# Kernel tuning notes

Measured on AMD Instinct MI355X. Metric: run time of the kernel, lower is better.

Reference implementation:

```python
import jax, jax.numpy as jnp
import numpy as np

N_NODES = 100000
N_GRAPHS = 512
HID = 128
IN_DIM = 128
OUT_DIM = 10
N_EDGES = 1600000


def gcn_conv(x, src, dst, W, b, n):
    # PyG GCNConv: add self-loops, symmetric normalization D^-1/2 (A+I) D^-1/2, then linear.
    h = x @ W  # [N, H]
    deg = jnp.zeros((n,), h.dtype).at[dst].add(1.0) + 1.0  # +1 self-loop
    dinv = jax.lax.rsqrt(deg)
    norm = dinv[src] * dinv[dst]  # [E]
    agg = jnp.zeros_like(h).at[dst].add(h[src] * norm[:, None])
    agg = agg + h * (dinv * dinv)[:, None]  # self-loop messages
    return agg + b


def setup_inputs() -> dict:
    key = jax.random.key(0)
    ks = jax.random.split(key, 12)
    x = jax.random.normal(ks[0], (N_NODES, IN_DIM), jnp.float32)
    edge_index = jax.random.randint(ks[1], (2, N_EDGES), 0, N_NODES)
    batch = jnp.sort(jax.random.randint(ks[2], (N_NODES,), 0, N_GRAPHS))
    def lin(k, fan_in, shape):
        bound = 1.0 / np.sqrt(fan_in)
        return jax.random.uniform(k, shape, jnp.float32, -bound, bound)
    W1 = lin(ks[3], IN_DIM, (IN_DIM, HID)); b1 = lin(ks[4], IN_DIM, (HID,))
    W2 = lin(ks[5], HID, (HID, HID)); b2 = lin(ks[6], HID, (HID,))
    W3 = lin(ks[7], HID, (HID, HID)); b3 = lin(ks[8], HID, (HID,))
    Wc1 = lin(ks[9], 2 * HID, (2 * HID, HID)); bc1 = lin(ks[9], 2 * HID, (HID,))
    Wc2 = lin(ks[10], HID, (HID, OUT_DIM)); bc2 = lin(ks[11], HID, (OUT_DIM,))
    return {"x": x, "edge_index": edge_index, "batch": batch,
            "W1": W1, "b1": b1, "W2": W2, "b2": b2, "W3": W3, "b3": b3,
            "Wc1": Wc1, "bc1": bc1, "Wc2": Wc2, "bc2": bc2}


def reference(x, edge_index, batch, W1, b1, W2, b2, W3, b3, Wc1, bc1, Wc2, bc2):
    src, dst = edge_index[0], edge_index[1]
    n = x.shape[0]
    h = jax.nn.relu(gcn_conv(x, src, dst, W1, b1, n))
    h = jax.nn.relu(gcn_conv(h, src, dst, W2, b2, n))
    h = gcn_conv(h, src, dst, W3, b3, n)  # no relu after last conv
    # global mean pool
    sums = jax.ops.segment_sum(h, batch, num_segments=N_GRAPHS)
    cnt = jax.ops.segment_sum(jnp.ones((n,), h.dtype), batch, num_segments=N_GRAPHS)
    mean = sums / jnp.maximum(cnt, 1.0)[:, None]
    # global max pool
    mx = jax.ops.segment_max(h, batch, num_segments=N_GRAPHS)
    mx = jnp.where(jnp.isfinite(mx), mx, 0.0)
    g = jnp.concatenate([mean, mx], axis=1)  # [G, 2H]
    g = jax.nn.relu(g @ Wc1 + bc1)
    return g @ Wc2 + bc2
```

## Files before the change

kernel.cpp:

```cpp
#include <hip/hip_runtime.h>

#define H 128
#define CAP 64
#define CSRB 4096

typedef __attribute__((ext_vector_type(8))) short bf16x8;
typedef __attribute__((ext_vector_type(4))) float f32x4;

__device__ __forceinline__ unsigned short f2bf(float f) {
  unsigned u = __float_as_uint(f);
  unsigned r = u + 0x7FFFu + ((u >> 16) & 1u);
  return (unsigned short)(r >> 16);
}
__device__ __forceinline__ float bf2f(unsigned short s) {
  return __uint_as_float(((unsigned)s) << 16);
}

__global__ __launch_bounds__(256) void fat_setup_csr(
    const int* __restrict__ src, const int* __restrict__ dst,
    int* __restrict__ cursor, int* __restrict__ csr_src,
    int ne, int range,
    const float* __restrict__ x,
    const float* __restrict__ W1, const float* __restrict__ W2, const float* __restrict__ W3,
    unsigned short* __restrict__ Xb, unsigned short* __restrict__ Wt,
    int n, int totalX4) {
  if (blockIdx.x < CSRB) {
    int r = blockIdx.x & 7;
    int slice = blockIdx.x >> 3;
    const int slices = CSRB / 8;
    int ne4 = ne / 4;
    int chunk4 = (ne4 + slices - 1) / slices;
    int beg4 = slice * chunk4;
    int end4 = beg4 + chunk4; if (end4 > ne4) end4 = ne4;
    int lo = r * range;
    int hi = lo + range;
    for (int e4 = beg4 + threadIdx.x; e4 < end4; e4 += 256) {
      int e = e4 * 4;
      int4 d = *(const int4*)(dst + e);
      if (d.x >= lo && d.x < hi) { int p = atomicAdd(&cursor[d.x], 1); if (p < CAP) csr_src[(size_t)d.x * CAP + p] = src[e + 0]; }
      if (d.y >= lo && d.y < hi) { int p = atomicAdd(&cursor[d.y], 1); if (p < CAP) csr_src[(size_t)d.y * CAP + p] = src[e + 1]; }
      if (d.z >= lo && d.z < hi) { int p = atomicAdd(&cursor[d.z], 1); if (p < CAP) csr_src[(size_t)d.z * CAP + p] = src[e + 2]; }
      if (d.w >= lo && d.w < hi) { int p = atomicAdd(&cursor[d.w], 1); if (p < CAP) csr_src[(size_t)d.w * CAP + p] = src[e + 3]; }
    }
    if (r == 0 && slice == 0) {
      int base = ne4 * 4;
      int t = base + threadIdx.x;
      if (t < ne) {
        int d = dst[t];
        int p = atomicAdd(&cursor[d], 1);
        if (p < CAP) csr_src[(size_t)d * CAP + p] = src[t];
      }
    }
    return;
  }
  long long i = (long long)(blockIdx.x - CSRB) * 256 + threadIdx.x;
  if (i < totalX4) {
    float4 v = *(const float4*)(x + i * 4);
    ushort4 o;
    o.x = f2bf(v.x); o.y = f2bf(v.y); o.z = f2bf(v.z); o.w = f2bf(v.w);
    *(ushort4*)(Xb + i * 4) = o;
    return;
  }
  i -= totalX4;
  if (i < 3 * H * H) {
    int w = (int)(i >> 14);
    int rem = (int)i & (H * H - 1);
    int c = rem >> 7;
    int k = rem & 127;
    const float* W = (w == 0) ? W1 : (w == 1) ? W2 : W3;
    Wt[i] = f2bf(W[(size_t)k * H + c]);
  }
}

__global__ void dinv_gstart(const int* __restrict__ deg, float* __restrict__ dinv,
                            const int* __restrict__ batch, int* __restrict__ g_start,
                            int n, int G) {
  int i = blockIdx.x * blockDim.x + threadIdx.x;
  if (i >= n) return;
  dinv[i] = rsqrtf((float)(deg[i] + 1));
  int b = batch[i];
  int prev = (i == 0) ? -1 : batch[i - 1];
  for (int g = prev + 1; g <= b; ++g) g_start[g] = i;
  if (i == n - 1) {
    for (int g = b + 1; g <= G; ++g) g_start[g] = n;
  }
}

#define SWLD 136
__global__ __launch_bounds__(256) void gemm_mfma(
    const unsigned short* __restrict__ Ab, const unsigned short* __restrict__ Wt,
    const float* __restrict__ dinv, unsigned short* __restrict__ outb, int n) {
  __shared__ unsigned short sW[H * SWLD];
  int tid = threadIdx.x;
  {
    int c = tid >> 1, hh = tid & 1;
    const int4* s = (const int4*)(Wt + (size_t)c * H + hh * 64);
    int4* d = (int4*)(sW + (size_t)c * SWLD + hh * 64);
#pragma unroll
    for (int i = 0; i < 8; ++i) d[i] = s[i];
  }
  __syncthreads();

  int wave = tid >> 6;
  int lane = tid & 63;
  int m = lane & 15;
  int quad = lane >> 4;
  int row = blockIdx.x * 64 + wave * 16 + m;
  bool rv = row < n;

  f32x4 acc[8];
#pragma unroll
  for (int t = 0; t < 8; ++t) acc[t] = (f32x4){0.f, 0.f, 0.f, 0.f};

  const unsigned short* arow = Ab + (size_t)(rv ? row : 0) * H;
#pragma unroll
  for (int k0 = 0; k0 < H; k0 += 32) {
    bf16x8 af;
    if (rv) af = *(const bf16x8*)(arow + k0 + quad * 8);
    else    af = (bf16x8){0, 0, 0, 0, 0, 0, 0, 0};
#pragma unroll
    for (int ct = 0; ct < 8; ++ct) {
      bf16x8 bfr = *(const bf16x8*)(sW + (size_t)(ct * 16 + m) * SWLD + k0 + quad * 8);
      acc[ct] = __builtin_amdgcn_mfma_f32_16x16x32_bf16(af, bfr, acc[ct], 0, 0, 0);
    }
  }

  int orow0 = blockIdx.x * 64 + wave * 16 + quad * 4;
#pragma unroll
  for (int r = 0; r < 4; ++r) {
    int orow = orow0 + r;
    if (orow < n) {
      float dv = dinv[orow];
      unsigned short* o = outb + (size_t)orow * H + m;
#pragma unroll
      for (int ct = 0; ct < 8; ++ct) o[ct * 16] = f2bf(acc[ct][r] * dv);
    }
  }
}

template <bool RELU, bool OUTF32>
__global__ __launch_bounds__(256) void aggregate_bf(
    const unsigned short* __restrict__ hs, const int* __restrict__ deg,
    const int* __restrict__ csr_src, const float* __restrict__ dinv,
    const float* __restrict__ b, void* __restrict__ outv, int n) {
  int node = blockIdx.x * 8 + (threadIdx.x >> 5);
  if (node >= n) return;
  int c = (threadIdx.x & 31) << 2;
  int dg = deg[node];
  int beg  = node * CAP;
  int end8 = beg + (dg & ~7);
  int end  = beg + dg;

  ushort4 sv = *(const ushort4*)(hs + (size_t)node * H + c);
  float4 acc;
  acc.x = bf2f(sv.x); acc.y = bf2f(sv.y); acc.z = bf2f(sv.z); acc.w = bf2f(sv.w);

  for (int k = beg; k < end8; k += 8) {
    int4 ca = *(const int4*)(csr_src + k);
    int4 cb = *(const int4*)(csr_src + k + 4);
    ushort4 v0 = *(const ushort4*)(hs + (size_t)ca.x * H + c);
    ushort4 v1 = *(const ushort4*)(hs + (size_t)ca.y * H + c);
    ushort4 v2 = *(const ushort4*)(hs + (size_t)ca.z * H + c);
    ushort4 v3 = *(const ushort4*)(hs + (size_t)ca.w * H + c);
    ushort4 v4 = *(const ushort4*)(hs + (size_t)cb.x * H + c);
    ushort4 v5 = *(const ushort4*)(hs + (size_t)cb.y * H + c);
    ushort4 v6 = *(const ushort4*)(hs + (size_t)cb.z * H + c);
    ushort4 v7 = *(const ushort4*)(hs + (size_t)cb.w * H + c);
    acc.x += ((bf2f(v0.x) + bf2f(v1.x)) + (bf2f(v2.x) + bf2f(v3.x))) +
             ((bf2f(v4.x) + bf2f(v5.x)) + (bf2f(v6.x) + bf2f(v7.x)));
    acc.y += ((bf2f(v0.y) + bf2f(v1.y)) + (bf2f(v2.y) + bf2f(v3.y))) +
             ((bf2f(v4.y) + bf2f(v5.y)) + (bf2f(v6.y) + bf2f(v7.y)));
    acc.z += ((bf2f(v0.z) + bf2f(v1.z)) + (bf2f(v2.z) + bf2f(v3.z))) +
             ((bf2f(v4.z) + bf2f(v5.z)) + (bf2f(v6.z) + bf2f(v7.z)));
    acc.w += ((bf2f(v0.w) + bf2f(v1.w)) + (bf2f(v2.w) + bf2f(v3.w))) +
             ((bf2f(v4.w) + bf2f(v5.w)) + (bf2f(v6.w) + bf2f(v7.w)));
  }
  for (int k = end8; k < end; ++k) {
    int s = csr_src[k];
    ushort4 v = *(const ushort4*)(hs + (size_t)s * H + c);
    acc.x += bf2f(v.x); acc.y += bf2f(v.y);
    acc.z += bf2f(v.z); acc.w += bf2f(v.w);
  }

  float dv = dinv[node];
  float4 bb = *(const float4*)(b + c);
  float4 o;
  o.x = fmaf(acc.x, dv, bb.x);
  o.y = fmaf(acc.y, dv, bb.y);
  o.z = fmaf(acc.z, dv, bb.z);
  o.w = fmaf(acc.w, dv, bb.w);
  if (RELU) {
    o.x = fmaxf(o.x, 0.f); o.y = fmaxf(o.y, 0.f);
    o.z = fmaxf(o.z, 0.f); o.w = fmaxf(o.w, 0.f);
  }
  if (OUTF32) {
    *(float4*)((float*)outv + (size_t)node * H + c) = o;
  } else {
    ushort4 ob;
    ob.x = f2bf(o.x); ob.y = f2bf(o.y); ob.z = f2bf(o.z); ob.w = f2bf(o.w);
    *(ushort4*)((unsigned short*)outv + (size_t)node * H + c) = ob;
  }
}

__global__ __launch_bounds__(256) void pool2(
    const float* __restrict__ h, const int* __restrict__ g_start,
    float* __restrict__ gmean, float* __restrict__ gmax, int n) {
  __shared__ float ssum[16][64];
  __shared__ float smax[16][64];
  int g = blockIdx.x >> 1;
  int half = blockIdx.x & 1;
  int beg = g_start[g];
  int end = g_start[g + 1];
  int q = threadIdx.x >> 4;
  int c = (threadIdx.x & 15) << 2;
  int cg = half * 64 + c;

  float4 s = make_float4(0.f, 0.f, 0.f, 0.f);
  float4 m = make_float4(-INFINITY, -INFINITY, -INFINITY, -INFINITY);
  for (int node = beg + q; node < end; node += 16) {
    float4 v = *(const float4*)(h + (size_t)node * H + cg);
    s.x += v.x; s.y += v.y; s.z += v.z; s.w += v.w;
    m.x = fmaxf(m.x, v.x); m.y = fmaxf(m.y, v.y);
    m.z = fmaxf(m.z, v.z); m.w = fmaxf(m.w, v.w);
  }
  *(float4*)&ssum[q][c] = s;
  *(float4*)&smax[q][c] = m;
  __syncthreads();

  int cnt = end - beg;
  int t = threadIdx.x;
  if (t < 64) {
    float tot = 0.f;
#pragma unroll
    for (int qq = 0; qq < 16; ++qq) tot += ssum[qq][t];
    gmean[(size_t)g * H + half * 64 + t] = tot / fmaxf((float)cnt, 1.0f);
  } else if (t < 128) {
    int cc = t - 64;
    float mx = -INFINITY;
#pragma unroll
    for (int qq = 0; qq < 16; ++qq) mx = fmaxf(mx, smax[qq][cc]);
    gmax[(size_t)g * H + half * 64 + cc] = (cnt == 0) ? 0.0f : mx;
  }
}

__global__ __launch_bounds__(128) void classify_kernel(
    const float* __restrict__ gmean, const float* __restrict__ gmax,
    const float* __restrict__ Wc1, const float* __restrict__ bc1,
    const float* __restrict__ Wc2, const float* __restrict__ bc2,
    float* __restrict__ out) {
  __shared__ float gv[2 * H];
  __shared__ float hid[H];
  int gid = blockIdx.x;
  int t = threadIdx.x;
  gv[t] = gmean[(size_t)gid * H + t];
  gv[H + t] = gmax[(size_t)gid * H + t];
  __syncthreads();
  float acc = 0.f;
#pragma unroll 8
  for (int k = 0; k < 2 * H; ++k) acc = fmaf(gv[k], Wc1[(size_t)k * H + t], acc);
  hid[t] = fmaxf(acc + bc1[t], 0.f);
  __syncthreads();
  if (t < 10) {
    float a2 = 0.f;
    for (int j = 0; j < H; ++j) a2 = fmaf(hid[j], Wc2[(size_t)j * 10 + t], a2);
    out[(size_t)gid * 10 + t] = a2 + bc2[t];
  }
}

extern "C" void kernel_launch(void* const* d_in, const int* in_sizes, int n_in,
                              void* d_out, int out_size, void* d_ws, size_t ws_size,
                              hipStream_t stream) {
  const float* x    = (const float*)d_in[0];
  const int* ei     = (const int*)d_in[1];
  const int* batch  = (const int*)d_in[2];
  const float* W1   = (const float*)d_in[3];
  const float* b1   = (const float*)d_in[4];
  const float* W2   = (const float*)d_in[5];
  const float* b2   = (const float*)d_in[6];
  const float* W3   = (const float*)d_in[7];
  const float* b3   = (const float*)d_in[8];
  const float* Wc1  = (const float*)d_in[9];
  const float* bc1  = (const float*)d_in[10];
  const float* Wc2  = (const float*)d_in[11];
  const float* bc2  = (const float*)d_in[12];
  float* out = (float*)d_out;

  const int n  = in_sizes[2];
  const int ne = in_sizes[1] / 2;
  const int G  = 512;
  const size_t NFb = (size_t)n * H;

  const int* src = ei;
  const int* dst = ei + ne;

  unsigned short* P_bf = (unsigned short*)d_ws;
  unsigned short* Q_bf = P_bf + NFb;
  float*          F2f  = (float*)(Q_bf + NFb);
  unsigned short* Xb   = (unsigned short*)F2f;
  int* csr_src = (int*)(F2f + NFb);
  const size_t csr_cap = (size_t)n * CAP;
  char* p = (char*)(csr_src + csr_cap);
  int*            cursor   = (int*)p;            p += (size_t)n * 4;
  float*          dinv     = (float*)p;          p += (size_t)n * 4;
  int*            g_start  = (int*)p;            p += (size_t)(G + 1) * 4;
  float*          gmean    = (float*)p;          p += (size_t)G * H * 4;
  float*          gmax     = (float*)p;          p += (size_t)G * H * 4;
  p = (char*)(((uintptr_t)p + 255) & ~(uintptr_t)255);
  unsigned short* Wt       = (unsigned short*)p; p += (size_t)3 * H * H * 2;

  hipMemsetAsync(cursor, 0, (size_t)n * 4, stream);

  {
    int totalX4 = n * H / 4;
    long long setup_items = (long long)totalX4 + 3 * H * H;
    int setup_blocks = (int)((setup_items + 255) / 256);
    int range = (n + 7) / 8;
    fat_setup_csr<<<CSRB + setup_blocks, 256, 0, stream>>>(
        src, dst, cursor, csr_src, ne, range,
        x, W1, W2, W3, Xb, Wt, n, totalX4);
  }
  dinv_gstart<<<(n + 255) / 256, 256, 0, stream>>>(cursor, dinv, batch, g_start, n, G);

  const int tile_grid = (n + 63) / 64;
  const int node_grid = (n + 7) / 8;

  gemm_mfma<<<tile_grid, 256, 0, stream>>>(Xb, Wt, dinv, Q_bf, n);
  aggregate_bf<true, false><<<node_grid, 256, 0, stream>>>(Q_bf, cursor, csr_src, dinv, b1, P_bf, n);

  gemm_mfma<<<tile_grid, 256, 0, stream>>>(P_bf, Wt + H * H, dinv, Q_bf, n);
  aggregate_bf<true, false><<<node_grid, 256, 0, stream>>>(Q_bf, cursor, csr_src, dinv, b2, P_bf, n);

  gemm_mfma<<<tile_grid, 256, 0, stream>>>(P_bf, Wt + 2 * H * H, dinv, Q_bf, n);
  aggregate_bf<false, true><<<node_grid, 256, 0, stream>>>(Q_bf, cursor, csr_src, dinv, b3, F2f, n);

  pool2<<<2 * G, 256, 0, stream>>>(F2f, g_start, gmean, gmax, n);
  classify_kernel<<<G, 128, 0, stream>>>(gmean, gmax, Wc1, bc1, Wc2, bc2, out);
}
```

Baseline: 464.6 us.

## Drop dinv/g_start kernel and fuse pooling with classifier

Removes the dinv_gstart kernel. dinv is now recomputed inline from the degree array with rsqrtf in the GEMM epilogue and in the aggregation kernel. Graph boundaries are found by binary search over the sorted batch array. Pooling and the classifier MLP are merged into one kernel per graph, so there are two fewer launches and no gmean/gmax round-trip through global memory. In exchange, one block now covers all 128 channels of a graph instead of two half-blocks, and the classifier uses only half of the threads.

```diff
diff --git a/kernel.cpp b/kernel.cpp
--- a/kernel.cpp
+++ b/kernel.cpp
@@ -72,24 +72,10 @@
   }
 }
 
-__global__ void dinv_gstart(const int* __restrict__ deg, float* __restrict__ dinv,
-                            const int* __restrict__ batch, int* __restrict__ g_start,
-                            int n, int G) {
-  int i = blockIdx.x * blockDim.x + threadIdx.x;
-  if (i >= n) return;
-  dinv[i] = rsqrtf((float)(deg[i] + 1));
-  int b = batch[i];
-  int prev = (i == 0) ? -1 : batch[i - 1];
-  for (int g = prev + 1; g <= b; ++g) g_start[g] = i;
-  if (i == n - 1) {
-    for (int g = b + 1; g <= G; ++g) g_start[g] = n;
-  }
-}
-
 #define SWLD 136
 __global__ __launch_bounds__(256) void gemm_mfma(
     const unsigned short* __restrict__ Ab, const unsigned short* __restrict__ Wt,
-    const float* __restrict__ dinv, unsigned short* __restrict__ outb, int n) {
+    const int* __restrict__ deg, unsigned short* __restrict__ outb, int n) {
   __shared__ unsigned short sW[H * SWLD];
   int tid = threadIdx.x;
   {
@@ -130,7 +116,7 @@
   for (int r = 0; r < 4; ++r) {
     int orow = orow0 + r;
     if (orow < n) {
-      float dv = dinv[orow];
+      float dv = rsqrtf((float)(deg[orow] + 1));
       unsigned short* o = outb + (size_t)orow * H + m;
 #pragma unroll
       for (int ct = 0; ct < 8; ++ct) o[ct * 16] = f2bf(acc[ct][r] * dv);
@@ -141,7 +127,7 @@
 template <bool RELU, bool OUTF32>
 __global__ __launch_bounds__(256) void aggregate_bf(
     const unsigned short* __restrict__ hs, const int* __restrict__ deg,
-    const int* __restrict__ csr_src, const float* __restrict__ dinv,
+    const int* __restrict__ csr_src,
     const float* __restrict__ b, void* __restrict__ outv, int n) {
   int node = blockIdx.x * 8 + (threadIdx.x >> 5);
   if (node >= n) return;
@@ -182,7 +168,7 @@
     acc.z += bf2f(v.z); acc.w += bf2f(v.w);
   }
 
-  float dv = dinv[node];
+  float dv = rsqrtf((float)(dg + 1));
   float4 bb = *(const float4*)(b + c);
   float4 o;
   o.x = fmaf(acc.x, dv, bb.x);
@@ -202,23 +188,34 @@
   }
 }
 
-__global__ __launch_bounds__(256) void pool2(
-    const float* __restrict__ h, const int* __restrict__ g_start,
-    float* __restrict__ gmean, float* __restrict__ gmax, int n) {
-  __shared__ float ssum[16][64];
-  __shared__ float smax[16][64];
-  int g = blockIdx.x >> 1;
-  int half = blockIdx.x & 1;
-  int beg = g_start[g];
-  int end = g_start[g + 1];
-  int q = threadIdx.x >> 4;
-  int c = (threadIdx.x & 15) << 2;
-  int cg = half * 64 + c;
-
+__global__ __launch_bounds__(256) void pool_classify(
+    const float* __restrict__ h, const int* __restrict__ batch,
+    const float* __restrict__ Wc1, const float* __restrict__ bc1,
+    const float* __restrict__ Wc2, const float* __restrict__ bc2,
+    float* __restrict__ out, int n) {
+  __shared__ float ssum[8][H];
+  __shared__ float smax[8][H];
+  __shared__ float gv[2 * H];
+  __shared__ float hid[H];
+  __shared__ int bounds[2];
+  int g = blockIdx.x;
+  int tid = threadIdx.x;
+
+  if (tid < 2) {
+    int target = g + tid;
+    int lo = 0, hi = n;
+    while (lo < hi) { int mid = (lo + hi) >> 1; if (batch[mid] < target) lo = mid + 1; else hi = mid; }
+    bounds[tid] = lo;
+  }
+  __syncthreads();
+  int beg = bounds[0], end = bounds[1];
+
+  int q = tid >> 5;
+  int c = (tid & 31) << 2;
   float4 s = make_float4(0.f, 0.f, 0.f, 0.f);
   float4 m = make_float4(-INFINITY, -INFINITY, -INFINITY, -INFINITY);
-  for (int node = beg + q; node < end; node += 16) {
-    float4 v = *(const float4*)(h + (size_t)node * H + cg);
+  for (int node = beg + q; node < end; node += 8) {
+    float4 v = *(const float4*)(h + (size_t)node * H + c);
     s.x += v.x; s.y += v.y; s.z += v.z; s.w += v.w;
     m.x = fmaxf(m.x, v.x); m.y = fmaxf(m.y, v.y);
     m.z = fmaxf(m.z, v.z); m.w = fmaxf(m.w, v.w);
@@ -228,42 +225,31 @@
   __syncthreads();
 
   int cnt = end - beg;
-  int t = threadIdx.x;
-  if (t < 64) {
+  if (tid < H) {
     float tot = 0.f;
 #pragma unroll
-    for (int qq = 0; qq < 16; ++qq) tot += ssum[qq][t];
-    gmean[(size_t)g * H + half * 64 + t] = tot / fmaxf((float)cnt, 1.0f);
-  } else if (t < 128) {
-    int cc = t - 64;
+    for (int qq = 0; qq < 8; ++qq) tot += ssum[qq][tid];
+    gv[tid] = tot / fmaxf((float)cnt, 1.0f);
+  } else {
+    int cc = tid - H;
     float mx = -INFINITY;
 #pragma unroll
-    for (int qq = 0; qq < 16; ++qq) mx = fmaxf(mx, smax[qq][cc]);
-    gmax[(size_t)g * H + half * 64 + cc] = (cnt == 0) ? 0.0f : mx;
-  }
-}
-
-__global__ __launch_bounds__(128) void classify_kernel(
-    const float* __restrict__ gmean, const float* __restrict__ gmax,
-    const float* __restrict__ Wc1, const float* __restrict__ bc1,
-    const float* __restrict__ Wc2, const float* __restrict__ bc2,
-    float* __restrict__ out) {
-  __shared__ float gv[2 * H];
-  __shared__ float hid[H];
-  int gid = blockIdx.x;
-  int t = threadIdx.x;
-  gv[t] = gmean[(size_t)gid * H + t];
-  gv[H + t] = gmax[(size_t)gid * H + t];
-  __syncthreads();
-  float acc = 0.f;
+    for (int qq = 0; qq < 8; ++qq) mx = fmaxf(mx, smax[qq][cc]);
+    gv[H + cc] = (cnt == 0) ? 0.0f : mx;
+  }
+  __syncthreads();
+
+  if (tid < H) {
+    float acc = 0.f;
 #pragma unroll 8
-  for (int k = 0; k < 2 * H; ++k) acc = fmaf(gv[k], Wc1[(size_t)k * H + t], acc);
-  hid[t] = fmaxf(acc + bc1[t], 0.f);
-  __syncthreads();
-  if (t < 10) {
+    for (int k = 0; k < 2 * H; ++k) acc = fmaf(gv[k], Wc1[(size_t)k * H + tid], acc);
+    hid[tid] = fmaxf(acc + bc1[tid], 0.f);
+  }
+  __syncthreads();
+  if (tid < 10) {
     float a2 = 0.f;
-    for (int j = 0; j < H; ++j) a2 = fmaf(hid[j], Wc2[(size_t)j * 10 + t], a2);
-    out[(size_t)gid * 10 + t] = a2 + bc2[t];
+    for (int j = 0; j < H; ++j) a2 = fmaf(hid[j], Wc2[(size_t)j * 10 + tid], a2);
+    out[(size_t)g * 10 + tid] = a2 + bc2[tid];
   }
 }
 
@@ -301,10 +287,6 @@
   const size_t csr_cap = (size_t)n * CAP;
   char* p = (char*)(csr_src + csr_cap);
   int*            cursor   = (int*)p;            p += (size_t)n * 4;
-  float*          dinv     = (float*)p;          p += (size_t)n * 4;
-  int*            g_start  = (int*)p;            p += (size_t)(G + 1) * 4;
-  float*          gmean    = (float*)p;          p += (size_t)G * H * 4;
-  float*          gmax     = (float*)p;          p += (size_t)G * H * 4;
   p = (char*)(((uintptr_t)p + 255) & ~(uintptr_t)255);
   unsigned short* Wt       = (unsigned short*)p; p += (size_t)3 * H * H * 2;
 
@@ -319,20 +301,18 @@
         src, dst, cursor, csr_src, ne, range,
         x, W1, W2, W3, Xb, Wt, n, totalX4);
   }
-  dinv_gstart<<<(n + 255) / 256, 256, 0, stream>>>(cursor, dinv, batch, g_start, n, G);
 
   const int tile_grid = (n + 63) / 64;
   const int node_grid = (n + 7) / 8;
 
-  gemm_mfma<<<tile_grid, 256, 0, stream>>>(Xb, Wt, dinv, Q_bf, n);
-  aggregate_bf<true, false><<<node_grid, 256, 0, stream>>>(Q_bf, cursor, csr_src, dinv, b1, P_bf, n);
-
-  gemm_mfma<<<tile_grid, 256, 0, stream>>>(P_bf, Wt + H * H, dinv, Q_bf, n);
-  aggregate_bf<true, false><<<node_grid, 256, 0, stream>>>(Q_bf, cursor, csr_src, dinv, b2, P_bf, n);
-
-  gemm_mfma<<<tile_grid, 256, 0, stream>>>(P_bf, Wt + 2 * H * H, dinv, Q_bf, n);
-  aggregate_bf<false, true><<<node_grid, 256, 0, stream>>>(Q_bf, cursor, csr_src, dinv, b3, F2f, n);
-
-  pool2<<<2 * G, 256, 0, stream>>>(F2f, g_start, gmean, gmax, n);
-  classify_kernel<<<G, 128, 0, stream>>>(gmean, gmax, Wc1, bc1, Wc2, bc2, out);
-}
+  gemm_mfma<<<tile_grid, 256, 0, stream>>>(Xb, Wt, cursor, Q_bf, n);
+  aggregate_bf<true, false><<<node_grid, 256, 0, stream>>>(Q_bf, cursor, csr_src, b1, P_bf, n);
+
+  gemm_mfma<<<tile_grid, 256, 0, stream>>>(P_bf, Wt + H * H, cursor, Q_bf, n);
+  aggregate_bf<true, false><<<node_grid, 256, 0, stream>>>(Q_bf, cursor, csr_src, b2, P_bf, n);
+
+  gemm_mfma<<<tile_grid, 256, 0, stream>>>(P_bf, Wt + 2 * H * H, cursor, Q_bf, n);
+  aggregate_bf<false, true><<<node_grid, 256, 0, stream>>>(Q_bf, cursor, csr_src, b3, F2f, n);
+
+  pool_classify<<<G, 256, 0, stream>>>(F2f, batch, Wc1, bc1, Wc2, bc2, out, n);
+}
```

Result: no change. 461.0 us (-0.8%).
